# Performance work log

Measured on AMD Instinct MI355X. Metric: run time of the kernel, lower is better.

The kernel has to match this reference:

```python
import jax, jax.numpy as jnp
import numpy as np

Q_MAX = 127.0  # symmetric int8 range

def setup_inputs() -> dict:
    key = jax.random.key(0)
    k1, k2, k3, k4 = jax.random.split(key, 4)
    B, S, K, N = 4, 2048, 4096, 4096
    inp = jax.random.normal(k1, (B, S, K), dtype=jnp.float32)
    # int8 weight in [-127, 127], stored via randint(0,255)-127 per spec
    qweight = (jax.random.randint(k2, (N, K), 0, 255) - 127).astype(jnp.int8)
    # per-out-channel weight dequant scales (small positive)
    wparams = (jax.random.uniform(k3, (N,), dtype=jnp.float32) * 0.02 + 0.001)
    bias = jax.random.normal(k4, (N,), dtype=jnp.float32) * 0.1
    return {"inp": inp, "qweight": qweight, "wparams": wparams, "bias": bias}

def reference(inp, qweight, wparams, bias):
    # inp: [B, S, K] float32; qweight: [N, K] int8; wparams: [N]; bias: [N]
    B, S, K = inp.shape
    x = inp.reshape(B * S, K)
    # qntz: per-row symmetric absmax quantization of the activation to int8
    a_scale = jnp.max(jnp.abs(x), axis=1, keepdims=True) / Q_MAX  # [M, 1]
    qinp = jnp.clip(jnp.round(x / a_scale), -Q_MAX, Q_MAX).astype(jnp.int8)  # [M, K]
    d = jax.lax.dot_general(qinp, qweight.T, (((1,), (0,)), ((), ())),
                            preferred_element_type=jnp.int32)  # [M, N]
    # dqntz: scale by per-row act scale and per-col weight scale, add bias
    out = d.astype(jnp.float32) * a_scale * wparams[None, :] + bias[None, :]
    return out.reshape(B, S, -1)
```

## Files before the change

### kernel.cpp

```cpp
#include <hip/hip_runtime.h>
#include <hip/hip_bf16.h>


using int32x4 = __attribute__((ext_vector_type(4))) int;

#define QMAXF 127.0f

__global__ __launch_bounds__(256) void repack_weights(
    const int* __restrict__ w, signed char* __restrict__ w8, int total)
{
    bool is32 = true;
#pragma unroll
    for (int i = 0; i < 16; ++i) {
        int v = w[i];
        is32 = is32 && (v >= -127 && v <= 127);
    }

    const int t = blockIdx.x * blockDim.x + threadIdx.x;
    const int nth = gridDim.x * blockDim.x;
    const int chunks = total / 16;

    if (is32) {
        for (int c = t; c < chunks; c += nth) {
            const int32x4* src = reinterpret_cast<const int32x4*>(w + (size_t)c * 16);
            int32x4 a0 = src[0], a1 = src[1], a2 = src[2], a3 = src[3];
            int32x4 o;
            o[0] = (a0[0] & 0xff) | ((a0[1] & 0xff) << 8) | ((a0[2] & 0xff) << 16) | ((a0[3] & 0xff) << 24);
            o[1] = (a1[0] & 0xff) | ((a1[1] & 0xff) << 8) | ((a1[2] & 0xff) << 16) | ((a1[3] & 0xff) << 24);
            o[2] = (a2[0] & 0xff) | ((a2[1] & 0xff) << 8) | ((a2[2] & 0xff) << 16) | ((a2[3] & 0xff) << 24);
            o[3] = (a3[0] & 0xff) | ((a3[1] & 0xff) << 8) | ((a3[2] & 0xff) << 16) | ((a3[3] & 0xff) << 24);
            reinterpret_cast<int32x4*>(w8)[c] = o;
        }
    } else {
        const int32x4* src = reinterpret_cast<const int32x4*>(w);
        int32x4* dst = reinterpret_cast<int32x4*>(w8);
        for (int c = t; c < chunks; c += nth) dst[c] = src[c];
    }
}

__global__ __launch_bounds__(256) void quant_rows(
    const float* __restrict__ x, signed char* __restrict__ q,
    float* __restrict__ scale, int K)
{
    const int row = blockIdx.x;
    const int t = threadIdx.x;
    const float4* xr = reinterpret_cast<const float4*>(x + (size_t)row * K);

    float4 v[4];
    float m = 0.f;
#pragma unroll
    for (int i = 0; i < 4; ++i) {
        v[i] = xr[t + i * 256];
        m = fmaxf(m, fmaxf(fmaxf(fabsf(v[i].x), fabsf(v[i].y)),
                           fmaxf(fabsf(v[i].z), fabsf(v[i].w))));
    }
#pragma unroll
    for (int off = 32; off >= 1; off >>= 1)
        m = fmaxf(m, __shfl_xor(m, off, 64));
    __shared__ float wmax[4];
    const int wave = t >> 6;
    if ((t & 63) == 0) wmax[wave] = m;
    __syncthreads();
    m = fmaxf(fmaxf(wmax[0], wmax[1]), fmaxf(wmax[2], wmax[3]));

    const float s   = m / QMAXF;
    const float inv = (m > 0.f) ? (QMAXF / m) : 0.f;
    if (t == 0) scale[row] = s;

    int* qr = reinterpret_cast<int*>(q + (size_t)row * K);
#pragma unroll
    for (int i = 0; i < 4; ++i) {
        const float* f = reinterpret_cast<const float*>(&v[i]);
        unsigned int packed = 0;
#pragma unroll
        for (int j = 0; j < 4; ++j) {
            int qi = __float2int_rn(f[j] * inv);
            qi = qi > 127 ? 127 : (qi < -127 ? -127 : qi);
            packed |= ((unsigned int)(qi & 0xff)) << (8 * j);
        }
        qr[t + i * 256] = (int)packed;
    }
}

#define BM 256
#define BN 256
#define BKB 64
#define NBUF 4

__device__ __forceinline__ void async_copy16(const void* g, void* lds) {
    __builtin_amdgcn_global_load_lds(
        (const __attribute__((address_space(1))) void*)g,
        (__attribute__((address_space(3))) void*)lds, 16, 0, 0);
}

__global__ __launch_bounds__(512, 2) void gemm_i8_dequant_rp(
    const signed char* __restrict__ A,
    const signed char* __restrict__ B,
    const float* __restrict__ a_scale,
    const float* __restrict__ wparams,
    const float* __restrict__ bias,
    float* __restrict__ out,
    int M, int N, int K)
{
    __shared__ __align__(16) signed char lds[NBUF * 32768];

    const int t    = threadIdx.x;
    const int lane = t & 63;
    const int wave = t >> 6;
    const int wr   = wave >> 2;
    const int wc   = wave & 3;

    const int nwg = gridDim.x;
    const int cpx = nwg >> 3;
    const int swz = (blockIdx.x & 7) * cpx + (blockIdx.x >> 3);
    const int nbx = N / BN;
    const int rowBase = (swz / nbx) * BM;
    const int colBase = (swz % nbx) * BN;

    const int r15 = lane & 15;
    const int ksl = lane >> 4;

    int32x4 acc[8][4] = {};
    const int NT = K / BKB;

    const signed char* gA0 = A + (size_t)(rowBase + wave * 16 + r15)       * K + ksl * 16;
    const signed char* gA1 = A + (size_t)(rowBase + (8 + wave) * 16 + r15) * K + ksl * 16;
    const signed char* gB0 = B + (size_t)(colBase + wave * 16 + r15)       * K + ksl * 16;
    const signed char* gB1 = B + (size_t)(colBase + (8 + wave) * 16 + r15) * K + ksl * 16;

    auto stageA = [&](int tile) {
        signed char* L = lds + (tile & (NBUF - 1)) * 32768;
        const size_t kt = (size_t)tile * BKB;
        async_copy16(gA0 + kt, L + wave * 1024);
        async_copy16(gA1 + kt, L + (8 + wave) * 1024);
    };
    auto stageB = [&](int tile) {
        signed char* L = lds + (tile & (NBUF - 1)) * 32768 + 16384;
        const size_t kt = (size_t)tile * BKB;
        async_copy16(gB0 + kt, L + wave * 1024);
        async_copy16(gB1 + kt, L + (8 + wave) * 1024);
    };
    auto ldFrags = [&](int tile, int32x4 (&fa)[8], int32x4 (&fb)[4]) {
        const signed char* Ab = lds + (tile & (NBUF - 1)) * 32768;
        const signed char* Bb = Ab + 16384;
#pragma unroll
        for (int mm = 0; mm < 8; ++mm)
            fa[mm] = *reinterpret_cast<const int32x4*>(
                Ab + (wr * 8 + mm) * 1024 + lane * 16);
#pragma unroll
        for (int nn = 0; nn < 4; ++nn)
            fb[nn] = *reinterpret_cast<const int32x4*>(
                Bb + (wc * 4 + nn) * 1024 + lane * 16);
    };
    auto mfmaAll = [&](const int32x4 (&fa)[8], const int32x4 (&fb)[4]) {
        __builtin_amdgcn_s_setprio(1);
#pragma unroll
        for (int mm = 0; mm < 8; ++mm)
#pragma unroll
            for (int nn = 0; nn < 4; ++nn)
                acc[mm][nn] = __builtin_amdgcn_mfma_i32_16x16x64_i8(
                    fa[mm], fb[nn], acc[mm][nn], 0, 0, 0);
        __builtin_amdgcn_s_setprio(0);
    };

    int32x4 rA0[8], rB0[4], rA1[8], rB1[4];

    stageA(0); stageB(0);
    stageA(1); stageB(1);
    stageA(2); stageB(2);
    stageA(3); stageB(3);
    asm volatile("s_waitcnt vmcnt(8)" ::: "memory");
    __builtin_amdgcn_s_barrier();
    ldFrags(0, rA0, rB0);
    asm volatile("s_waitcnt lgkmcnt(0)" ::: "memory");
    __builtin_amdgcn_s_barrier();

    for (int tt = 0; tt < NT - 4; tt += 2) {
        stageA(tt + 4);
        ldFrags(tt + 1, rA1, rB1);
        stageB(tt + 4);
        mfmaAll(rA0, rB0);
        asm volatile("s_waitcnt vmcnt(8) lgkmcnt(0)" ::: "memory");
        __builtin_amdgcn_s_barrier();

        stageA(tt + 5);
        ldFrags(tt + 2, rA0, rB0);
        stageB(tt + 5);
        mfmaAll(rA1, rB1);
        asm volatile("s_waitcnt vmcnt(8) lgkmcnt(0)" ::: "memory");
        __builtin_amdgcn_s_barrier();
    }

    ldFrags(NT - 3, rA1, rB1);
    mfmaAll(rA0, rB0);
    asm volatile("s_waitcnt vmcnt(4) lgkmcnt(0)" ::: "memory");
    __builtin_amdgcn_s_barrier();
    ldFrags(NT - 2, rA0, rB0);
    mfmaAll(rA1, rB1);
    asm volatile("s_waitcnt vmcnt(0) lgkmcnt(0)" ::: "memory");
    __builtin_amdgcn_s_barrier();
    ldFrags(NT - 1, rA1, rB1);
    mfmaAll(rA0, rB0);
    mfmaAll(rA1, rB1);

#pragma unroll
    for (int mm = 0; mm < 8; ++mm) {
        const int rb = rowBase + wr * 128 + mm * 16 + ksl * 4;
        float asc[4];
#pragma unroll
        for (int r = 0; r < 4; ++r) asc[r] = a_scale[rb + r];
#pragma unroll
        for (int nn = 0; nn < 4; ++nn) {
            const int col = colBase + wc * 64 + nn * 16 + r15;
            const float wp = wparams[col];
            const float bs = bias[col];
#pragma unroll
            for (int r = 0; r < 4; ++r) {
                out[(size_t)(rb + r) * N + col] =
                    (float)acc[mm][nn][r] * asc[r] * wp + bs;
            }
        }
    }
}

extern "C" void kernel_launch(void* const* d_in, const int* in_sizes, int n_in,
                              void* d_out, int out_size, void* d_ws, size_t ws_size,
                              hipStream_t stream) {
    const float* inp     = (const float*)d_in[0];
    const int*   qw_raw  = (const int*)d_in[1];
    const float* wparams = (const float*)d_in[2];
    const float* bias    = (const float*)d_in[3];
    float*       out     = (float*)d_out;

    const int N = in_sizes[2];
    const int K = in_sizes[1] / N;
    const int M = in_sizes[0] / K;

    signed char* qinp    = (signed char*)d_ws;
    float*       a_scale = (float*)((char*)d_ws + (size_t)M * K);
    size_t off_w8 = (size_t)M * K + (((size_t)M * sizeof(float) + 255) & ~(size_t)255);
    signed char* w8      = (signed char*)((char*)d_ws + off_w8);

    repack_weights<<<2048, 256, 0, stream>>>(qw_raw, w8, N * K);
    quant_rows<<<M, 256, 0, stream>>>(inp, qinp, a_scale, K);

    const int nwg = (M / BM) * (N / BN);
    gemm_i8_dequant_rp<<<nwg, 512, 0, stream>>>(
        qinp, w8, a_scale, wparams, bias, out, M, N, K);
}
```

Measured before the change: 203.7 us.

## Restructure GEMM pipeline to prefetch depth three with scheduling barriers

The main loop now prefetches three tiles ahead instead of four, merging the A and B async copies into one stage call. Each step waits with vmcnt(4) and uses sched_barrier-fenced s_barriers so the compiler cannot move work across synchronisation points. LDS fragment addresses are precomputed per wave. The aim is tighter control of instruction scheduling and less waiting per barrier. The cost is less latency hiding, since only two tiles are in flight while one is being consumed.

```diff
diff --git a/kernel.cpp b/kernel.cpp
--- a/kernel.cpp
+++ b/kernel.cpp
@@ -93,7 +93,19 @@
         (__attribute__((address_space(3))) void*)lds, 16, 0, 0);
 }
 
-__global__ __launch_bounds__(512, 2) void gemm_i8_dequant_rp(
+#define BARF do {                                         \
+    __builtin_amdgcn_sched_barrier(0);                    \
+    asm volatile("" ::: "memory");                        \
+    __builtin_amdgcn_s_barrier();                         \
+    asm volatile("" ::: "memory");                        \
+    __builtin_amdgcn_sched_barrier(0);                    \
+} while (0)
+
+#define LGKM0 asm volatile("s_waitcnt lgkmcnt(0)" ::: "memory")
+#define VM4   asm volatile("s_waitcnt vmcnt(4)" ::: "memory")
+#define VM0   asm volatile("s_waitcnt vmcnt(0)" ::: "memory")
+
+__global__ __launch_bounds__(512, 2) void gemm_i8_dequant_ov(
     const signed char* __restrict__ A,
     const signed char* __restrict__ B,
     const float* __restrict__ a_scale,
@@ -128,29 +140,23 @@
     const signed char* gB0 = B + (size_t)(colBase + wave * 16 + r15)       * K + ksl * 16;
     const signed char* gB1 = B + (size_t)(colBase + (8 + wave) * 16 + r15) * K + ksl * 16;
 
-    auto stageA = [&](int tile) {
+    auto stage = [&](int tile) {
         signed char* L = lds + (tile & (NBUF - 1)) * 32768;
         const size_t kt = (size_t)tile * BKB;
         async_copy16(gA0 + kt, L + wave * 1024);
         async_copy16(gA1 + kt, L + (8 + wave) * 1024);
-    };
-    auto stageB = [&](int tile) {
-        signed char* L = lds + (tile & (NBUF - 1)) * 32768 + 16384;
-        const size_t kt = (size_t)tile * BKB;
-        async_copy16(gB0 + kt, L + wave * 1024);
-        async_copy16(gB1 + kt, L + (8 + wave) * 1024);
+        async_copy16(gB0 + kt, L + 16384 + wave * 1024);
+        async_copy16(gB1 + kt, L + 16384 + (8 + wave) * 1024);
     };
     auto ldFrags = [&](int tile, int32x4 (&fa)[8], int32x4 (&fb)[4]) {
-        const signed char* Ab = lds + (tile & (NBUF - 1)) * 32768;
-        const signed char* Bb = Ab + 16384;
+        const signed char* Ab = lds + (tile & (NBUF - 1)) * 32768 + wr * 8192 + lane * 16;
+        const signed char* Bb = lds + (tile & (NBUF - 1)) * 32768 + 16384 + wc * 4096 + lane * 16;
 #pragma unroll
         for (int mm = 0; mm < 8; ++mm)
-            fa[mm] = *reinterpret_cast<const int32x4*>(
-                Ab + (wr * 8 + mm) * 1024 + lane * 16);
+            fa[mm] = *reinterpret_cast<const int32x4*>(Ab + mm * 1024);
 #pragma unroll
         for (int nn = 0; nn < 4; ++nn)
-            fb[nn] = *reinterpret_cast<const int32x4*>(
-                Bb + (wc * 4 + nn) * 1024 + lane * 16);
+            fb[nn] = *reinterpret_cast<const int32x4*>(Bb + nn * 1024);
     };
     auto mfmaAll = [&](const int32x4 (&fa)[8], const int32x4 (&fb)[4]) {
         __builtin_amdgcn_s_setprio(1);
@@ -163,45 +169,38 @@
         __builtin_amdgcn_s_setprio(0);
     };
 
-    int32x4 rA0[8], rB0[4], rA1[8], rB1[4];
-
-    stageA(0); stageB(0);
-    stageA(1); stageB(1);
-    stageA(2); stageB(2);
-    stageA(3); stageB(3);
-    asm volatile("s_waitcnt vmcnt(8)" ::: "memory");
-    __builtin_amdgcn_s_barrier();
-    ldFrags(0, rA0, rB0);
-    asm volatile("s_waitcnt lgkmcnt(0)" ::: "memory");
-    __builtin_amdgcn_s_barrier();
-
-    for (int tt = 0; tt < NT - 4; tt += 2) {
-        stageA(tt + 4);
-        ldFrags(tt + 1, rA1, rB1);
-        stageB(tt + 4);
-        mfmaAll(rA0, rB0);
-        asm volatile("s_waitcnt vmcnt(8) lgkmcnt(0)" ::: "memory");
-        __builtin_amdgcn_s_barrier();
-
-        stageA(tt + 5);
-        ldFrags(tt + 2, rA0, rB0);
-        stageB(tt + 5);
-        mfmaAll(rA1, rB1);
-        asm volatile("s_waitcnt vmcnt(8) lgkmcnt(0)" ::: "memory");
-        __builtin_amdgcn_s_barrier();
-    }
-
-    ldFrags(NT - 3, rA1, rB1);
-    mfmaAll(rA0, rB0);
-    asm volatile("s_waitcnt vmcnt(4) lgkmcnt(0)" ::: "memory");
-    __builtin_amdgcn_s_barrier();
-    ldFrags(NT - 2, rA0, rB0);
-    mfmaAll(rA1, rB1);
-    asm volatile("s_waitcnt vmcnt(0) lgkmcnt(0)" ::: "memory");
-    __builtin_amdgcn_s_barrier();
-    ldFrags(NT - 1, rA1, rB1);
-    mfmaAll(rA0, rB0);
-    mfmaAll(rA1, rB1);
+    int32x4 cA[8], cB[4], nA[8], nB[4];
+
+    stage(0); stage(1); stage(2);
+    VM4;
+    BARF;
+    ldFrags(0, cA, cB);
+
+    for (int tt = 0; tt + 1 < NT - 3; tt += 2) {
+        stage(tt + 3);
+        ldFrags(tt + 1, nA, nB);
+        mfmaAll(cA, cB);
+        VM4; LGKM0; BARF;
+
+        stage(tt + 4);
+        ldFrags(tt + 2, cA, cB);
+        mfmaAll(nA, nB);
+        VM4; LGKM0; BARF;
+    }
+
+    stage(NT - 1);
+    ldFrags(NT - 3, nA, nB);
+    mfmaAll(cA, cB);
+    VM4; LGKM0; BARF;
+
+    ldFrags(NT - 2, cA, cB);
+    mfmaAll(nA, nB);
+    VM0; LGKM0; BARF;
+
+    ldFrags(NT - 1, nA, nB);
+    mfmaAll(cA, cB);
+
+    mfmaAll(nA, nB);
 
 #pragma unroll
     for (int mm = 0; mm < 8; ++mm) {
@@ -245,6 +244,6 @@
     quant_rows<<<M, 256, 0, stream>>>(inp, qinp, a_scale, K);
 
     const int nwg = (M / BM) * (N / BN);
-    gemm_i8_dequant_rp<<<nwg, 512, 0, stream>>>(
+    gemm_i8_dequant_ov<<<nwg, 512, 0, stream>>>(
         qinp, w8, a_scale, wparams, bias, out, M, N, K);
 }
```

After: 203.5 us. No clear change (-0.1%).
